# Kernel tuning notes

Measured on AMD Instinct MI355X. Metric: run time of the kernel, lower is better.

## Reference

```python
import jax, jax.numpy as jnp
import numpy as np

H = 50  # hidden size hard-coded in the torch module


def _lstm_layer(x, W_ih, W_hh, b_ih, b_hh):
    """x: [B, T, D_in] -> outputs [B, T, H]. PyTorch gate order: i, f, g, o."""
    B = x.shape[0]
    # precompute input projection for all timesteps: [B, T, 4H]
    x_proj = jnp.einsum('btd,gd->btg', x, W_ih) + b_ih + b_hh
    x_proj = jnp.swapaxes(x_proj, 0, 1)  # time-major [T, B, 4H]

    def step(carry, xt):
        h, c = carry
        gates = xt + h @ W_hh.T  # [B, 4H]
        i, f, g, o = jnp.split(gates, 4, axis=-1)
        c = jax.nn.sigmoid(f) * c + jax.nn.sigmoid(i) * jnp.tanh(g)
        h = jax.nn.sigmoid(o) * jnp.tanh(c)
        return (h, c), h

    h0 = jnp.zeros((B, H), dtype=x.dtype)
    c0 = jnp.zeros((B, H), dtype=x.dtype)
    (_, _), hs = jax.lax.scan(step, (h0, c0), x_proj)
    return jnp.swapaxes(hs, 0, 1)  # [B, T, H]


def setup_inputs() -> dict:
    key = jax.random.key(0)
    ks = jax.random.split(key, 11)
    B, T = 4096, 512
    s = 1.0 / np.sqrt(H)  # torch LSTM init scale
    return {
        'x': jax.random.normal(ks[0], (B, T, 1), dtype=jnp.float32),
        'W_ih0': jax.random.normal(ks[1], (4 * H, 1), dtype=jnp.float32) * s,
        'W_hh0': jax.random.normal(ks[2], (4 * H, H), dtype=jnp.float32) * s,
        'b_ih0': jax.random.normal(ks[3], (4 * H,), dtype=jnp.float32) * s,
        'b_hh0': jax.random.normal(ks[4], (4 * H,), dtype=jnp.float32) * s,
        'W_ih1': jax.random.normal(ks[5], (4 * H, H), dtype=jnp.float32) * s,
        'W_hh1': jax.random.normal(ks[6], (4 * H, H), dtype=jnp.float32) * s,
        'b_ih1': jax.random.normal(ks[7], (4 * H,), dtype=jnp.float32) * s,
        'b_hh1': jax.random.normal(ks[8], (4 * H,), dtype=jnp.float32) * s,
        'W_fc': jax.random.normal(ks[9], (1, H), dtype=jnp.float32) * s,
        'b_fc': jax.random.normal(ks[10], (1,), dtype=jnp.float32) * s,
    }


def reference(x, W_ih0, W_hh0, b_ih0, b_hh0, W_ih1, W_hh1, b_ih1, b_hh1, W_fc, b_fc):
    h1 = _lstm_layer(x, W_ih0, W_hh0, b_ih0, b_hh0)   # [B, T, H]
    h2 = _lstm_layer(h1, W_ih1, W_hh1, b_ih1, b_hh1)  # [B, T, H]
    last = h2[:, -1, :]                                # [B, H]
    return last @ W_fc.T + b_fc                        # [B, 1]
```

## Files before the change

kernel.cpp:

```cpp
#include <hip/hip_runtime.h>


#define TT 512
#define HH 50
#define BT 16
#define NTHR 1024
#define L2E 1.44269504f

typedef _Float16 half8 __attribute__((ext_vector_type(8)));
typedef float floatx4 __attribute__((ext_vector_type(4)));

static __device__ __forceinline__ float fexp2(float x) { return __builtin_amdgcn_exp2f(x); }
static __device__ __forceinline__ float frcp(float x)  { return __builtin_amdgcn_rcpf(x); }

static __device__ __forceinline__ float cell_update(float gi, float gf, float gg,
                                                    float go, float& c) {
    float Ei = fexp2(gi);
    float Eg = fexp2(gg);
    float Ef = fexp2(gf);
    float p1 = (1.0f + Ei) * (1.0f + Eg);
    float fe = 1.0f + Ef;
    float R  = frcp(fe * p1);
    c = R * (c * p1 + (1.0f - Eg) * fe);
    float cl = fminf(fmaxf(c, -18.0f), 18.0f);
    float Eo = fexp2(go);
    float Ec = fexp2(cl * (-2.0f * L2E));
    float Ro = frcp((1.0f + Eo) * (1.0f + Ec));
    return (1.0f - Ec) * Ro;
}

#define MFMA(a, b, c) __builtin_amdgcn_mfma_f32_16x16x32_f16((a), (b), (c), 0, 0, 0)

template<int NJ>
static __device__ __forceinline__ void run_l0(
    int tbase, int ln, _Float16 (*Hf)[2048], const float* xs,
    const float* __restrict__ W_ih0, const float* __restrict__ W_hh0,
    const float* __restrict__ b_ih0, const float* __restrict__ b_hh0)
{
    const int m = ln & 15, q = ln >> 4;
    const float GSC[4] = { -L2E, -L2E, -2.0f * L2E, -L2E };

    half8 a0[NJ][2];
    float cc0[NJ][4], bw0[NJ][4], c[NJ];
    int   widx[NJ];
#pragma unroll
    for (int j = 0; j < NJ; ++j) {
        const int  tau  = tbase + j;
        const int  uA   = 4 * tau + (m >> 2);
        const int  gA   = m & 3;
        const bool rokA = (uA < HH);
        const int  wrow = gA * HH + uA;
        const float sA  = GSC[gA];
#pragma unroll
        for (int ks = 0; ks < 2; ++ks) {
            half8 h8;
#pragma unroll
            for (int jj = 0; jj < 8; ++jj) {
                int k = ks * 32 + q * 8 + jj;
                float w = (rokA && k < HH) ? W_hh0[wrow * HH + k] : 0.f;
                h8[jj] = (_Float16)(sA * w);
            }
            a0[j][ks] = h8;
        }
        const int  uC = 4 * tau + q;
        const bool vC = (uC < HH);
#pragma unroll
        for (int g = 0; g < 4; ++g) {
            int rg = g * HH + (vC ? uC : 0);
            cc0[j][g] = vC ? GSC[g] * (b_ih0[rg] + b_hh0[rg]) : 0.f;
            bw0[j][g] = vC ? GSC[g] * W_ih0[rg] : 0.f;
        }
        const int kh = uC & 63;
        widx[j] = ((kh >> 5) * 64 + ((kh >> 3) & 3) * 16 + m) * 8 + (kh & 7);
        c[j] = 0.f;
    }

    __syncthreads();

    {
        const float xv = xs[m];
#pragma unroll
        for (int j = 0; j < NJ; ++j) {
            float h = cell_update(cc0[j][0] + bw0[j][0] * xv, cc0[j][1] + bw0[j][1] * xv,
                                  cc0[j][2] + bw0[j][2] * xv, cc0[j][3] + bw0[j][3] * xv,
                                  c[j]);
            Hf[1][widx[j]] = (_Float16)h;
        }
        __syncthreads();
    }

#define ITER0(ttv, P)                                                       \
    {                                                                       \
        half8 b0 = *(const half8*)&Hf[(P)][(0 * 64 + ln) * 8];              \
        half8 b1 = *(const half8*)&Hf[(P)][(1 * 64 + ln) * 8];              \
        const float xv = xs[(ttv) * BT + m];                                \
        floatx4 acc[NJ];                                                    \
        _Pragma("unroll")                                                   \
        for (int j = 0; j < NJ; ++j) {                                      \
            floatx4 a;                                                      \
            _Pragma("unroll")                                               \
            for (int g = 0; g < 4; ++g) a[g] = cc0[j][g] + bw0[j][g] * xv;  \
            a = MFMA(a0[j][0], b0, a);                                      \
            a = MFMA(a0[j][1], b1, a);                                      \
            acc[j] = a;                                                     \
        }                                                                   \
        _Pragma("unroll")                                                   \
        for (int j = 0; j < NJ; ++j) {                                      \
            float h = cell_update(acc[j][0], acc[j][1], acc[j][2], acc[j][3], c[j]); \
            Hf[(P) ^ 1][widx[j]] = (_Float16)h;                             \
        }                                                                   \
        __syncthreads();                                                    \
    }

    for (int k = 1; k <= 255; ++k) {
        ITER0(2 * k - 1, 1);
        ITER0(2 * k, 0);
    }
    ITER0(511, 1);
    __syncthreads();
#undef ITER0
}

template<int NJ>
static __device__ __forceinline__ void run_l1(
    int tbase, int ln, _Float16 (*Hf)[2048],
    const float* __restrict__ W_ih1, const float* __restrict__ W_hh1,
    const float* __restrict__ b_ih1, const float* __restrict__ b_hh1)
{
    const int m = ln & 15, q = ln >> 4;
    const float GSC[4] = { -L2E, -L2E, -2.0f * L2E, -L2E };

    half8 a1[NJ][4];
    float cc1[NJ][4], c[NJ];
    int   widx[NJ];
#pragma unroll
    for (int j = 0; j < NJ; ++j) {
        const int  tau  = tbase + j;
        const int  uA   = 4 * tau + (m >> 2);
        const int  gA   = m & 3;
        const bool rokA = (uA < HH);
        const int  wrow = gA * HH + uA;
        const float sA  = GSC[gA];
#pragma unroll
        for (int ks = 0; ks < 4; ++ks) {
            half8 h8;
#pragma unroll
            for (int jj = 0; jj < 8; ++jj) {
                int k = ks * 32 + q * 8 + jj;
                float w = 0.f;
                if (rokA) {
                    if (k < HH)                      w = W_ih1[wrow * HH + k];
                    else if (k >= 64 && k < 64 + HH) w = W_hh1[wrow * HH + (k - 64)];
                }
                h8[jj] = (_Float16)(sA * w);
            }
            a1[j][ks] = h8;
        }
        const int  uC = 4 * tau + q;
        const bool vC = (uC < HH);
#pragma unroll
        for (int g = 0; g < 4; ++g) {
            int rg = g * HH + (vC ? uC : 0);
            cc1[j][g] = vC ? GSC[g] * (b_ih1[rg] + b_hh1[rg]) : 0.f;
        }
        const int kh = uC & 63;
        widx[j] = ((kh >> 5) * 64 + ((kh >> 3) & 3) * 16 + m) * 8 + (kh & 7) + 1024;
        c[j] = 0.f;
    }

    __syncthreads();
    __syncthreads();

#define ITER1(P)                                                            \
    {                                                                       \
        half8 b0 = *(const half8*)&Hf[(P)][(0 * 64 + ln) * 8];              \
        half8 b1 = *(const half8*)&Hf[(P)][(1 * 64 + ln) * 8];              \
        half8 b2 = *(const half8*)&Hf[(P)][(2 * 64 + ln) * 8];              \
        half8 b3 = *(const half8*)&Hf[(P)][(3 * 64 + ln) * 8];              \
        floatx4 acc[NJ];                                                    \
        _Pragma("unroll")                                                   \
        for (int j = 0; j < NJ; ++j) {                                      \
            floatx4 a;                                                      \
            _Pragma("unroll")                                               \
            for (int g = 0; g < 4; ++g) a[g] = cc1[j][g];                   \
            a = MFMA(a1[j][0], b0, a);                                      \
            a = MFMA(a1[j][1], b1, a);                                      \
            a = MFMA(a1[j][2], b2, a);                                      \
            a = MFMA(a1[j][3], b3, a);                                      \
            acc[j] = a;                                                     \
        }                                                                   \
        _Pragma("unroll")                                                   \
        for (int j = 0; j < NJ; ++j) {                                      \
            float h = cell_update(acc[j][0], acc[j][1], acc[j][2], acc[j][3], c[j]); \
            Hf[(P) ^ 1][widx[j]] = (_Float16)h;                             \
        }                                                                   \
        __syncthreads();                                                    \
    }

    for (int k = 1; k <= 255; ++k) {
        ITER1(1);
        ITER1(0);
    }
    ITER1(1);
    ITER1(0);
#undef ITER1
}

__global__ __launch_bounds__(NTHR, 4) void lstm_mfma(
    const float* __restrict__ x,
    const float* __restrict__ W_ih0, const float* __restrict__ W_hh0,
    const float* __restrict__ b_ih0, const float* __restrict__ b_hh0,
    const float* __restrict__ W_ih1, const float* __restrict__ W_hh1,
    const float* __restrict__ b_ih1, const float* __restrict__ b_hh1,
    const float* __restrict__ W_fc,  const float* __restrict__ b_fc,
    float* __restrict__ out)
{
    __shared__ __align__(16) _Float16 Hf[2][2048];
    __shared__ float xs[TT * BT];

    const int tid = threadIdx.x;
    const int ln  = tid & 63;
    const int wv  = tid >> 6;
    const int b0g = blockIdx.x * BT;

    for (int i = tid; i < BT * TT; i += NTHR) {
        int b = i & 15, t = i >> 4;
        xs[t * BT + b] = x[(size_t)(b0g + b) * TT + t];
    }
    for (int i = tid; i < 2 * 2048; i += NTHR) ((_Float16*)Hf)[i] = (_Float16)0.f;

    if (wv < 8) {
        if (wv < 5)
            run_l0<2>(2 * wv, ln, Hf, xs, W_ih0, W_hh0, b_ih0, b_hh0);
        else
            run_l0<1>(10 + (wv - 5), ln, Hf, xs, W_ih0, W_hh0, b_ih0, b_hh0);
    } else {
        const int w = wv - 8;
        if (w < 3)
            run_l1<1>(w, ln, Hf, W_ih1, W_hh1, b_ih1, b_hh1);
        else
            run_l1<2>(3 + 2 * (w - 3), ln, Hf, W_ih1, W_hh1, b_ih1, b_hh1);
    }

    if (tid < BT) {
        float a = b_fc[0];
        for (int u = 0; u < HH; ++u) {
            int k = 64 + u;
            int idx = ((k >> 5) * 64 + ((k >> 3) & 3) * 16 + tid) * 8 + (k & 7);
            a = fmaf((float)Hf[1][idx], W_fc[u], a);
        }
        out[b0g + tid] = a;
    }
}

extern "C" void kernel_launch(void* const* d_in, const int* in_sizes, int n_in,
                              void* d_out, int out_size, void* d_ws, size_t ws_size,
                              hipStream_t stream) {
    const float* x     = (const float*)d_in[0];
    const float* W_ih0 = (const float*)d_in[1];
    const float* W_hh0 = (const float*)d_in[2];
    const float* b_ih0 = (const float*)d_in[3];
    const float* b_hh0 = (const float*)d_in[4];
    const float* W_ih1 = (const float*)d_in[5];
    const float* W_hh1 = (const float*)d_in[6];
    const float* b_ih1 = (const float*)d_in[7];
    const float* b_hh1 = (const float*)d_in[8];
    const float* W_fc  = (const float*)d_in[9];
    const float* b_fc  = (const float*)d_in[10];
    float* out = (float*)d_out;

    dim3 grid(4096 / BT);
    dim3 block(NTHR);
    lstm_mfma<<<grid, block, 0, stream>>>(x, W_ih0, W_hh0, b_ih0, b_hh0,
                                          W_ih1, W_hh1, b_ih1, b_hh1,
                                          W_fc, b_fc, out);
}
```

Before: 369.1 us.

## Fold bias and input term into MFMA and split layer buffers with rotating ring

Bias and the layer-0 input weight are packed into spare K columns (50, 51) of the weight fragments, with constant 1 and x_t written into the hidden-state buffer, so per-step accumulator initialisation becomes zero. Layer-0 and layer-1 state now live in separate buffers: a 4-deep ring for h1 and a double buffer for h2. Layer 1 prefetches h1 fragments into registers before the barrier. This removes per-step VALU FMAs and register arrays for bias terms, at the cost of fp16 precision on the bias and input values and a more intricate buffer-indexing pipeline.

```diff
diff --git a/kernel.cpp b/kernel.cpp
--- a/kernel.cpp
+++ b/kernel.cpp
@@ -31,9 +31,9 @@
 
 #define MFMA(a, b, c) __builtin_amdgcn_mfma_f32_16x16x32_f16((a), (b), (c), 0, 0, 0)
 
-template<int NJ>
+template<int NJ, bool WRITER>
 static __device__ __forceinline__ void run_l0(
-    int tbase, int ln, _Float16 (*Hf)[2048], const float* xs,
+    int tbase, int ln, _Float16 (*H1)[1024], const float* xs,
     const float* __restrict__ W_ih0, const float* __restrict__ W_hh0,
     const float* __restrict__ b_ih0, const float* __restrict__ b_hh0)
 {
@@ -41,7 +41,7 @@
     const float GSC[4] = { -L2E, -L2E, -2.0f * L2E, -L2E };
 
     half8 a0[NJ][2];
-    float cc0[NJ][4], bw0[NJ][4], c[NJ];
+    float c[NJ];
     int   widx[NJ];
 #pragma unroll
     for (int j = 0; j < NJ; ++j) {
@@ -57,20 +57,18 @@
 #pragma unroll
             for (int jj = 0; jj < 8; ++jj) {
                 int k = ks * 32 + q * 8 + jj;
-                float w = (rokA && k < HH) ? W_hh0[wrow * HH + k] : 0.f;
+                float w = 0.f;
+                if (rokA) {
+                    if (k < HH)       w = W_hh0[wrow * HH + k];
+                    else if (k == 50) w = b_ih0[wrow] + b_hh0[wrow];
+                    else if (k == 51) w = W_ih0[wrow];
+                }
                 h8[jj] = (_Float16)(sA * w);
             }
             a0[j][ks] = h8;
         }
-        const int  uC = 4 * tau + q;
-        const bool vC = (uC < HH);
-#pragma unroll
-        for (int g = 0; g < 4; ++g) {
-            int rg = g * HH + (vC ? uC : 0);
-            cc0[j][g] = vC ? GSC[g] * (b_ih0[rg] + b_hh0[rg]) : 0.f;
-            bw0[j][g] = vC ? GSC[g] * W_ih0[rg] : 0.f;
-        }
-        const int kh = uC & 63;
+        const int uC = 4 * tau + q;
+        const int kh = (uC < HH) ? uC : (uC + 2);
         widx[j] = ((kh >> 5) * 64 + ((kh >> 3) & 3) * 16 + m) * 8 + (kh & 7);
         c[j] = 0.f;
     }
@@ -81,49 +79,50 @@
         const float xv = xs[m];
 #pragma unroll
         for (int j = 0; j < NJ; ++j) {
-            float h = cell_update(cc0[j][0] + bw0[j][0] * xv, cc0[j][1] + bw0[j][1] * xv,
-                                  cc0[j][2] + bw0[j][2] * xv, cc0[j][3] + bw0[j][3] * xv,
-                                  c[j]);
-            Hf[1][widx[j]] = (_Float16)h;
+            const int  uC = 4 * (tbase + j) + q;
+            const bool vC = (uC < HH);
+            float g4[4];
+#pragma unroll
+            for (int g = 0; g < 4; ++g) {
+                int rg = g * HH + (vC ? uC : 0);
+                g4[g] = vC ? GSC[g] * ((b_ih0[rg] + b_hh0[rg]) + W_ih0[rg] * xv) : 0.f;
+            }
+            float h = cell_update(g4[0], g4[1], g4[2], g4[3], c[j]);
+            H1[0][widx[j]] = (_Float16)h;
+        }
+    }
+    __syncthreads();
+
+    const floatx4 ZERO = { 0.f, 0.f, 0.f, 0.f };
+    for (int s = 1; s <= 513; ++s) {
+        if (s <= 511) {
+            const _Float16* bufR = H1[(s - 1) & 3];
+            _Float16*       bufW = H1[s & 3];
+            half8 b0 = *(const half8*)&bufR[(0  + ln) * 8];
+            half8 b1 = *(const half8*)&bufR[(64 + ln) * 8];
+            floatx4 acc[NJ];
+#pragma unroll
+            for (int j = 0; j < NJ; ++j) {
+                floatx4 a = MFMA(a0[j][0], b0, ZERO);
+                acc[j] = MFMA(a0[j][1], b1, a);
+            }
+#pragma unroll
+            for (int j = 0; j < NJ; ++j) {
+                float h = cell_update(acc[j][0], acc[j][1], acc[j][2], acc[j][3], c[j]);
+                bufW[widx[j]] = (_Float16)h;
+            }
+            if (WRITER) {
+                if (ln < 16)
+                    bufW[(96 + ln) * 8 + 3] = (_Float16)xs[(s + 1) * BT + ln];
+            }
         }
         __syncthreads();
     }
-
-#define ITER0(ttv, P)                                                       \
-    {                                                                       \
-        half8 b0 = *(const half8*)&Hf[(P)][(0 * 64 + ln) * 8];              \
-        half8 b1 = *(const half8*)&Hf[(P)][(1 * 64 + ln) * 8];              \
-        const float xv = xs[(ttv) * BT + m];                                \
-        floatx4 acc[NJ];                                                    \
-        _Pragma("unroll")                                                   \
-        for (int j = 0; j < NJ; ++j) {                                      \
-            floatx4 a;                                                      \
-            _Pragma("unroll")                                               \
-            for (int g = 0; g < 4; ++g) a[g] = cc0[j][g] + bw0[j][g] * xv;  \
-            a = MFMA(a0[j][0], b0, a);                                      \
-            a = MFMA(a0[j][1], b1, a);                                      \
-            acc[j] = a;                                                     \
-        }                                                                   \
-        _Pragma("unroll")                                                   \
-        for (int j = 0; j < NJ; ++j) {                                      \
-            float h = cell_update(acc[j][0], acc[j][1], acc[j][2], acc[j][3], c[j]); \
-            Hf[(P) ^ 1][widx[j]] = (_Float16)h;                             \
-        }                                                                   \
-        __syncthreads();                                                    \
-    }
-
-    for (int k = 1; k <= 255; ++k) {
-        ITER0(2 * k - 1, 1);
-        ITER0(2 * k, 0);
-    }
-    ITER0(511, 1);
-    __syncthreads();
-#undef ITER0
 }
 
 template<int NJ>
 static __device__ __forceinline__ void run_l1(
-    int tbase, int ln, _Float16 (*Hf)[2048],
+    int tbase, int ln, _Float16 (*H1)[1024], _Float16 (*H2)[1024],
     const float* __restrict__ W_ih1, const float* __restrict__ W_hh1,
     const float* __restrict__ b_ih1, const float* __restrict__ b_hh1)
 {
@@ -131,7 +130,7 @@
     const float GSC[4] = { -L2E, -L2E, -2.0f * L2E, -L2E };
 
     half8 a1[NJ][4];
-    float cc1[NJ][4], c[NJ];
+    float c[NJ];
     int   widx[NJ];
 #pragma unroll
     for (int j = 0; j < NJ; ++j) {
@@ -150,60 +149,51 @@
                 float w = 0.f;
                 if (rokA) {
                     if (k < HH)                      w = W_ih1[wrow * HH + k];
+                    else if (k == 50)                w = b_ih1[wrow] + b_hh1[wrow];
                     else if (k >= 64 && k < 64 + HH) w = W_hh1[wrow * HH + (k - 64)];
                 }
                 h8[jj] = (_Float16)(sA * w);
             }
             a1[j][ks] = h8;
         }
-        const int  uC = 4 * tau + q;
-        const bool vC = (uC < HH);
-#pragma unroll
-        for (int g = 0; g < 4; ++g) {
-            int rg = g * HH + (vC ? uC : 0);
-            cc1[j][g] = vC ? GSC[g] * (b_ih1[rg] + b_hh1[rg]) : 0.f;
-        }
-        const int kh = uC & 63;
-        widx[j] = ((kh >> 5) * 64 + ((kh >> 3) & 3) * 16 + m) * 8 + (kh & 7) + 1024;
+        const int uC = 4 * tau + q;
+        const int kh = (uC < HH) ? uC : (uC + 2);
+        widx[j] = ((kh >> 5) * 64 + ((kh >> 3) & 3) * 16 + m) * 8 + (kh & 7);
         c[j] = 0.f;
     }
 
     __syncthreads();
     __syncthreads();
 
-#define ITER1(P)                                                            \
-    {                                                                       \
-        half8 b0 = *(const half8*)&Hf[(P)][(0 * 64 + ln) * 8];              \
-        half8 b1 = *(const half8*)&Hf[(P)][(1 * 64 + ln) * 8];              \
-        half8 b2 = *(const half8*)&Hf[(P)][(2 * 64 + ln) * 8];              \
-        half8 b3 = *(const half8*)&Hf[(P)][(3 * 64 + ln) * 8];              \
-        floatx4 acc[NJ];                                                    \
-        _Pragma("unroll")                                                   \
-        for (int j = 0; j < NJ; ++j) {                                      \
-            floatx4 a;                                                      \
-            _Pragma("unroll")                                               \
-            for (int g = 0; g < 4; ++g) a[g] = cc1[j][g];                   \
-            a = MFMA(a1[j][0], b0, a);                                      \
-            a = MFMA(a1[j][1], b1, a);                                      \
-            a = MFMA(a1[j][2], b2, a);                                      \
-            a = MFMA(a1[j][3], b3, a);                                      \
-            acc[j] = a;                                                     \
-        }                                                                   \
-        _Pragma("unroll")                                                   \
-        for (int j = 0; j < NJ; ++j) {                                      \
-            float h = cell_update(acc[j][0], acc[j][1], acc[j][2], acc[j][3], c[j]); \
-            Hf[(P) ^ 1][widx[j]] = (_Float16)h;                             \
-        }                                                                   \
-        __syncthreads();                                                    \
-    }
-
-    for (int k = 1; k <= 255; ++k) {
-        ITER1(1);
-        ITER1(0);
-    }
-    ITER1(1);
-    ITER1(0);
-#undef ITER1
+    half8 p0 = {}, p1 = {};
+    const floatx4 ZERO = { 0.f, 0.f, 0.f, 0.f };
+    for (int s = 1; s <= 513; ++s) {
+        if (s >= 2) {
+            const _Float16* h2R = H2[(s - 1) & 1];
+            _Float16*       h2W = H2[s & 1];
+            half8 b2 = *(const half8*)&h2R[(0  + ln) * 8];
+            half8 b3 = *(const half8*)&h2R[(64 + ln) * 8];
+            floatx4 acc[NJ];
+#pragma unroll
+            for (int j = 0; j < NJ; ++j) {
+                floatx4 a = MFMA(a1[j][0], p0, ZERO);
+                a = MFMA(a1[j][1], p1, a);
+                a = MFMA(a1[j][2], b2, a);
+                acc[j] = MFMA(a1[j][3], b3, a);
+            }
+#pragma unroll
+            for (int j = 0; j < NJ; ++j) {
+                float h = cell_update(acc[j][0], acc[j][1], acc[j][2], acc[j][3], c[j]);
+                h2W[widx[j]] = (_Float16)h;
+            }
+        }
+        {
+            const _Float16* h1R = H1[(s - 1) & 3];
+            p0 = *(const half8*)&h1R[(0  + ln) * 8];
+            p1 = *(const half8*)&h1R[(64 + ln) * 8];
+        }
+        __syncthreads();
+    }
 }
 
 __global__ __launch_bounds__(NTHR, 4) void lstm_mfma(
@@ -215,8 +205,9 @@
     const float* __restrict__ W_fc,  const float* __restrict__ b_fc,
     float* __restrict__ out)
 {
-    __shared__ __align__(16) _Float16 Hf[2][2048];
-    __shared__ float xs[TT * BT];
+    __shared__ __align__(16) _Float16 H1[4][1024];
+    __shared__ __align__(16) _Float16 H2[2][1024];
+    __shared__ float xs[(TT + 1) * BT];
 
     const int tid = threadIdx.x;
     const int ln  = tid & 63;
@@ -227,27 +218,36 @@
         int b = i & 15, t = i >> 4;
         xs[t * BT + b] = x[(size_t)(b0g + b) * TT + t];
     }
-    for (int i = tid; i < 2 * 2048; i += NTHR) ((_Float16*)Hf)[i] = (_Float16)0.f;
+    if (tid < BT) xs[TT * BT + tid] = 0.f;
+    for (int i = tid; i < 4 * 1024; i += NTHR) ((_Float16*)H1)[i] = (_Float16)0.f;
+    for (int i = tid; i < 2 * 1024; i += NTHR) ((_Float16*)H2)[i] = (_Float16)0.f;
+    __syncthreads();
+    if (tid < 16) {
+#pragma unroll
+        for (int r = 0; r < 4; ++r) H1[r][(96 + tid) * 8 + 2] = (_Float16)1.0f;
+        H1[0][(96 + tid) * 8 + 3] = (_Float16)xs[BT + tid];
+    }
 
     if (wv < 8) {
         if (wv < 5)
-            run_l0<2>(2 * wv, ln, Hf, xs, W_ih0, W_hh0, b_ih0, b_hh0);
+            run_l0<2, false>(2 * wv, ln, H1, xs, W_ih0, W_hh0, b_ih0, b_hh0);
+        else if (wv < 7)
+            run_l0<1, false>(10 + (wv - 5), ln, H1, xs, W_ih0, W_hh0, b_ih0, b_hh0);
         else
-            run_l0<1>(10 + (wv - 5), ln, Hf, xs, W_ih0, W_hh0, b_ih0, b_hh0);
+            run_l0<1, true>(12, ln, H1, xs, W_ih0, W_hh0, b_ih0, b_hh0);
     } else {
         const int w = wv - 8;
         if (w < 3)
-            run_l1<1>(w, ln, Hf, W_ih1, W_hh1, b_ih1, b_hh1);
+            run_l1<1>(w, ln, H1, H2, W_ih1, W_hh1, b_ih1, b_hh1);
         else
-            run_l1<2>(3 + 2 * (w - 3), ln, Hf, W_ih1, W_hh1, b_ih1, b_hh1);
+            run_l1<2>(3 + 2 * (w - 3), ln, H1, H2, W_ih1, W_hh1, b_ih1, b_hh1);
     }
 
     if (tid < BT) {
         float a = b_fc[0];
         for (int u = 0; u < HH; ++u) {
-            int k = 64 + u;
-            int idx = ((k >> 5) * 64 + ((k >> 3) & 3) * 16 + tid) * 8 + (k & 7);
-            a = fmaf((float)Hf[1][idx], W_fc[u], a);
+            int idx = ((u >> 5) * 64 + ((u >> 3) & 3) * 16 + tid) * 8 + (u & 7);
+            a = fmaf((float)H2[1][idx], W_fc[u], a);
         }
         out[b0g + tid] = a;
     }
```

Result: no change. 364.5 us (-1.2%).
